# Performance work log

Hardware: AMD Instinct MI355X
Metric: run time of the kernel (lower is better)

The kernel has to match this reference:

```python
import jax, jax.numpy as jnp
import numpy as np

N = 50000   # nodes
E = 800000  # edges
H = 3       # attention heads
IN_F = 128
HID = 128
NUM_CLASSES = 6
GAT_SLOPE = 0.2   # DGL GATConv internal leaky_relu slope
ACT_SLOPE = 0.01  # nn.LeakyReLU default


def setup_inputs() -> dict:
    key = jax.random.key(0)
    ks = jax.random.split(key, 24)
    s = 0.05
    inp = {
        "in_feat": jax.random.normal(ks[0], (N, IN_F), jnp.float32),
        "src": jax.random.randint(ks[1], (E,), 0, N, jnp.int32),
        "dst": jax.random.randint(ks[2], (E,), 0, N, jnp.int32),
        # GATConv 1: W (IN_F, H*HID), attn vectors (H, HID), bias (H*HID)
        "W1": jax.random.normal(ks[3], (IN_F, H * HID), jnp.float32) * s,
        "al1": jax.random.normal(ks[4], (H, HID), jnp.float32) * s,
        "ar1": jax.random.normal(ks[5], (H, HID), jnp.float32) * s,
        "b1": jnp.zeros((H * HID,), jnp.float32),
        # GATConv 2
        "W2": jax.random.normal(ks[6], (HID, H * HID), jnp.float32) * s,
        "al2": jax.random.normal(ks[7], (H, HID), jnp.float32) * s,
        "ar2": jax.random.normal(ks[8], (H, HID), jnp.float32) * s,
        "b2": jnp.zeros((H * HID,), jnp.float32),
    }
    # Dense MLP head lin1..lin4 (HID->HID) and lin5 (HID->NUM_CLASSES)
    for i in range(1, 5):
        inp[f"lw{i}"] = jax.random.normal(ks[8 + 2 * i], (HID, HID), jnp.float32) * s
        inp[f"lb{i}"] = jnp.zeros((HID,), jnp.float32)
    inp["lw5"] = jax.random.normal(ks[20], (HID, NUM_CLASSES), jnp.float32) * s
    inp["lb5"] = jnp.zeros((NUM_CLASSES,), jnp.float32)
    return inp


def gat_conv(x, src, dst, W, al, ar, b):
    # x: (N, F_in) -> out: (N, H, HID)
    h = (x @ W).reshape(N, H, HID)
    el = jnp.einsum('nhf,hf->nh', h, al)  # (N, H)
    er = jnp.einsum('nhf,hf->nh', h, ar)
    e = jax.nn.leaky_relu(el[src] + er[dst], GAT_SLOPE)  # (E, H)
    # edge softmax over incoming edges of each dst node
    m = jax.ops.segment_max(e, dst, num_segments=N)
    m = jnp.where(jnp.isfinite(m), m, 0.0)
    ex = jnp.exp(e - m[dst])
    denom = jax.ops.segment_sum(ex, dst, num_segments=N)
    alpha = ex / (denom[dst] + 1e-9)  # (E, H)
    out = jax.ops.segment_sum(alpha[:, :, None] * h[src], dst, num_segments=N)
    return out + b.reshape(1, H, HID)


def reference(in_feat, src, dst, W1, al1, ar1, b1, W2, al2, ar2, b2,
              lw1, lb1, lw2, lb2, lw3, lb3, lw4, lb4, lw5, lb5):
    act = lambda x: jax.nn.leaky_relu(x, ACT_SLOPE)
    h = act(gat_conv(in_feat, src, dst, W1, al1, ar1, b1)).mean(axis=1)
    h = act(gat_conv(h, src, dst, W2, al2, ar2, b2)).mean(axis=1)
    h = act(h @ lw1 + lb1)
    h = act(h @ lw2 + lb2)
    h = act(h @ lw3 + lb3)
    h = act(h @ lw4 + lb4)
    return h @ lw5 + lb5
```

## Files before the change

kernel.cpp:

```cpp
#include <hip/hip_runtime.h>
#include <hip/hip_bf16.h>


typedef __attribute__((ext_vector_type(8))) short short8;
typedef __attribute__((ext_vector_type(4))) float float4v;

__device__ inline short f2bf(float x) {
    union { float f; unsigned u; } v; v.f = x;
    unsigned r = v.u + 0x7FFFu + ((v.u >> 16) & 1u);
    return (short)(r >> 16);
}
__device__ inline float bf2f(short b) {
    union { float f; unsigned u; } v;
    v.u = ((unsigned)(unsigned short)b) << 16;
    return v.f;
}
__device__ inline float bfhi(unsigned u) {
    union { unsigned u; float f; } v; v.u = u & 0xffff0000u; return v.f;
}
__device__ inline float bflo(unsigned u) {
    union { unsigned u; float f; } v; v.u = u << 16; return v.f;
}
__device__ inline short8 zero8() { short8 z = {0,0,0,0,0,0,0,0}; return z; }

#define BM 128
#define BN 128
#define BK 32
#define LSTR 40
#define MSTR 136
#define MROWS 64

__global__ void prep_kernel(
    const float* __restrict__ in_feat, short* __restrict__ P1h,
    short* __restrict__ P1l, int n4, int cb, int wb,
    const int* __restrict__ dst, int* __restrict__ cnt, int E,
    const float* __restrict__ w1, const float* __restrict__ w2,
    const float* __restrict__ m1, const float* __restrict__ m2,
    const float* __restrict__ m3, const float* __restrict__ m4,
    const float* __restrict__ w5,
    short* __restrict__ w1h, short* __restrict__ w1l,
    short* __restrict__ w2h, short* __restrict__ w2l,
    short* __restrict__ m1h, short* __restrict__ m1l,
    short* __restrict__ m2h, short* __restrict__ m2l,
    short* __restrict__ m3h, short* __restrict__ m3l,
    short* __restrict__ m4h, short* __restrict__ m4l,
    short* __restrict__ w5h, short* __restrict__ w5l)
{
    int blk = blockIdx.x;
    if (blk < cb) {
        int i = blk * 256 + threadIdx.x;
        if (i >= n4) return;
        float4 v = *(const float4*)(in_feat + (size_t)i * 4);
        float xs[4] = {v.x, v.y, v.z, v.w};
        short hs[4], ls[4];
        #pragma unroll
        for (int j = 0; j < 4; ++j) {
            hs[j] = f2bf(xs[j]);
            ls[j] = f2bf(xs[j] - bf2f(hs[j]));
        }
        *(uint2*)(P1h + (size_t)i * 4) = *(uint2*)hs;
        *(uint2*)(P1l + (size_t)i * 4) = *(uint2*)ls;
    } else if (blk < cb + wb) {
        int j = (blk - cb) * 256 + threadIdx.x;
        const float* src; short* th; short* tl; int Nc, base;
        if      (j < 49152)  { src = w1; th = w1h; tl = w1l; Nc = 384; base = 0; }
        else if (j < 98304)  { src = w2; th = w2h; tl = w2l; Nc = 384; base = 49152; }
        else if (j < 114688) { src = m1; th = m1h; tl = m1l; Nc = 128; base = 98304; }
        else if (j < 131072) { src = m2; th = m2h; tl = m2l; Nc = 128; base = 114688; }
        else if (j < 147456) { src = m3; th = m3h; tl = m3l; Nc = 128; base = 131072; }
        else if (j < 163840) { src = m4; th = m4h; tl = m4l; Nc = 128; base = 147456; }
        else if (j < 164608) { src = w5; th = w5h; tl = w5l; Nc = 6;   base = 163840; }
        else return;
        int i = j - base;
        int k = i / Nc, c = i - k * Nc;
        float v = src[i];
        short h = f2bf(v);
        th[(size_t)c * 128 + k] = h;
        tl[(size_t)c * 128 + k] = f2bf(v - bf2f(h));
    } else {
        int e = (blk - cb - wb) * 256 + threadIdx.x;
        if (e < E) atomicAdd(&cnt[dst[e]], 1);
    }
}

__global__ __launch_bounds__(256) void gemm_mfma(
    const short* __restrict__ Ahi, const short* __restrict__ Alo,
    const short* __restrict__ Bth, const short* __restrict__ Btl,
    const float* __restrict__ bias,
    float* __restrict__ Cf, short* __restrict__ Chi, short* __restrict__ Clo,
    float* __restrict__ el, float* __restrict__ er,
    const float* __restrict__ al, const float* __restrict__ ar,
    int M, int Nc, int flags)
{
    __shared__ short Ah[BM * LSTR], Al_[BM * LSTR];
    __shared__ short Bh[BN * LSTR], Bl_[BN * LSTR];

    int tid = threadIdx.x, lane = tid & 63, wave = tid >> 6;
    int l15 = lane & 15, q = lane >> 4;
    int rowBase = blockIdx.y * BM, colBase = blockIdx.x * BN;

    float4v acc[2][8];
    #pragma unroll
    for (int mt = 0; mt < 2; ++mt)
        #pragma unroll
        for (int nt = 0; nt < 8; ++nt)
            acc[mt][nt] = (float4v){0.f, 0.f, 0.f, 0.f};

    for (int k0 = 0; k0 < 128; k0 += BK) {
        #pragma unroll
        for (int s = 0; s < 2; ++s) {
            int c = tid + s * 256;
            int r = c >> 2, kq = (c & 3) * 8;
            int gr = rowBase + r;
            short8 vh = zero8(), vl = zero8();
            if (gr < M) {
                vh = *(const short8*)(Ahi + (size_t)gr * 128 + k0 + kq);
                vl = *(const short8*)(Alo + (size_t)gr * 128 + k0 + kq);
            }
            *(short8*)&Ah[r * LSTR + kq]  = vh;
            *(short8*)&Al_[r * LSTR + kq] = vl;
            int gc = colBase + r;
            short8 wh = zero8(), wl = zero8();
            if (gc < Nc) {
                wh = *(const short8*)(Bth + (size_t)gc * 128 + k0 + kq);
                wl = *(const short8*)(Btl + (size_t)gc * 128 + k0 + kq);
            }
            *(short8*)&Bh[r * LSTR + kq]  = wh;
            *(short8*)&Bl_[r * LSTR + kq] = wl;
        }
        __syncthreads();

        short8 aH[2], aL2[2];
        #pragma unroll
        for (int mt = 0; mt < 2; ++mt) {
            int off = (wave * 32 + mt * 16 + l15) * LSTR + q * 8;
            aH[mt]  = *(short8*)&Ah[off];
            aL2[mt] = *(short8*)&Al_[off];
        }
        #pragma unroll
        for (int nt = 0; nt < 8; ++nt) {
            int off = (nt * 16 + l15) * LSTR + q * 8;
            short8 bH = *(short8*)&Bh[off];
            short8 bL = *(short8*)&Bl_[off];
            #pragma unroll
            for (int mt = 0; mt < 2; ++mt) {
                acc[mt][nt] = __builtin_amdgcn_mfma_f32_16x16x32_bf16(aH[mt], bH, acc[mt][nt], 0, 0, 0);
                acc[mt][nt] = __builtin_amdgcn_mfma_f32_16x16x32_bf16(aH[mt], bL, acc[mt][nt], 0, 0, 0);
                acc[mt][nt] = __builtin_amdgcn_mfma_f32_16x16x32_bf16(aL2[mt], bH, acc[mt][nt], 0, 0, 0);
            }
        }
        __syncthreads();
    }

    if (flags & 4) {
        const float* alh = al + colBase;
        const float* arh = ar + colBase;
        float pel[2][4] = {}, per_[2][4] = {};
        #pragma unroll
        for (int nt = 0; nt < 8; ++nt) {
            float av = alh[nt * 16 + l15];
            float rv = arh[nt * 16 + l15];
            #pragma unroll
            for (int mt = 0; mt < 2; ++mt)
                #pragma unroll
                for (int i = 0; i < 4; ++i) {
                    pel[mt][i]  += acc[mt][nt][i] * av;
                    per_[mt][i] += acc[mt][nt][i] * rv;
                }
        }
        #pragma unroll
        for (int mask = 1; mask < 16; mask <<= 1)
            #pragma unroll
            for (int mt = 0; mt < 2; ++mt)
                #pragma unroll
                for (int i = 0; i < 4; ++i) {
                    pel[mt][i]  += __shfl_xor(pel[mt][i], mask);
                    per_[mt][i] += __shfl_xor(per_[mt][i], mask);
                }
        if (l15 == 0) {
            #pragma unroll
            for (int mt = 0; mt < 2; ++mt)
                #pragma unroll
                for (int i = 0; i < 4; ++i) {
                    int r = rowBase + wave * 32 + mt * 16 + q * 4 + i;
                    if (r < M) {
                        el[r * 3 + blockIdx.x] = pel[mt][i];
                        er[r * 3 + blockIdx.x] = per_[mt][i];
                    }
                }
        }
    }

    #pragma unroll
    for (int mt = 0; mt < 2; ++mt) {
        #pragma unroll
        for (int nt = 0; nt < 8; ++nt) {
            int c = colBase + nt * 16 + l15;
            if (c >= Nc) continue;
            float bv = (flags & 1) ? bias[c] : 0.f;
            #pragma unroll
            for (int i = 0; i < 4; ++i) {
                int r = rowBase + wave * 32 + mt * 16 + q * 4 + i;
                if (r >= M) continue;
                float v = acc[mt][nt][i] + bv;
                if (flags & 2) v = (v < 0.f) ? 0.01f * v : v;
                if (flags & 8)  Cf[(size_t)r * Nc + c] = v;
                if (flags & 16) {
                    size_t idx = (flags & 64)
                        ? ((size_t)r * 128 + (size_t)(c - colBase)) * 3 + blockIdx.x
                        : (size_t)r * Nc + c;
                    short hh = f2bf(v);
                    Chi[idx] = hh;
                    if (flags & 32) Clo[idx] = f2bf(v - bf2f(hh));
                }
            }
        }
    }
}

__global__ __launch_bounds__(256) void mlp_fused(
    const short* __restrict__ Ph, const short* __restrict__ Pl,
    const short* __restrict__ w1h, const short* __restrict__ w1l,
    const short* __restrict__ w2h, const short* __restrict__ w2l,
    const short* __restrict__ w3h, const short* __restrict__ w3l,
    const short* __restrict__ w4h, const short* __restrict__ w4l,
    const short* __restrict__ w5h, const short* __restrict__ w5l,
    const float* __restrict__ b1, const float* __restrict__ b2,
    const float* __restrict__ b3, const float* __restrict__ b4,
    const float* __restrict__ b5,
    float* __restrict__ out, int M)
{
    __shared__ short AH[MROWS * MSTR], AL[MROWS * MSTR];
    __shared__ short WH[128 * LSTR], WL[128 * LSTR];

    int tid = threadIdx.x, lane = tid & 63, wave = tid >> 6;
    int l15 = lane & 15, q = lane >> 4;
    int rowBase = blockIdx.x * MROWS;

    #pragma unroll
    for (int s = 0; s < 4; ++s) {
        int idx = tid + s * 256;
        int r = idx >> 4, kq = (idx & 15) * 8;
        int gr = rowBase + r;
        short8 vh = zero8(), vl = zero8();
        if (gr < M) {
            vh = *(const short8*)(Ph + (size_t)gr * 128 + kq);
            vl = *(const short8*)(Pl + (size_t)gr * 128 + kq);
        }
        *(short8*)&AH[r * MSTR + kq] = vh;
        *(short8*)&AL[r * MSTR + kq] = vl;
    }

    const short* Whs[4] = {w1h, w2h, w3h, w4h};
    const short* Wls[4] = {w1l, w2l, w3l, w4l};
    const float* Bss[4] = {b1, b2, b3, b4};

    #pragma unroll
    for (int L = 0; L < 4; ++L) {
        float4v acc[8];
        #pragma unroll
        for (int nt = 0; nt < 8; ++nt)
            acc[nt] = (float4v){0.f, 0.f, 0.f, 0.f};

        for (int k0 = 0; k0 < 128; k0 += BK) {
            #pragma unroll
            for (int s = 0; s < 4; ++s) {
                int idx = tid + s * 256;
                int plane = idx >> 9, rem = idx & 511;
                int c = rem >> 2, kq = (rem & 3) * 8;
                short8 v = *(const short8*)((plane ? Wls[L] : Whs[L]) +
                                            (size_t)c * 128 + k0 + kq);
                *(short8*)&((plane ? WL : WH)[c * LSTR + kq]) = v;
            }
            __syncthreads();
            int offa = (wave * 16 + l15) * MSTR + k0 + q * 8;
            short8 aH  = *(short8*)&AH[offa];
            short8 aL2 = *(short8*)&AL[offa];
            #pragma unroll
            for (int nt = 0; nt < 8; ++nt) {
                int off = (nt * 16 + l15) * LSTR + q * 8;
                short8 bH = *(short8*)&WH[off];
                short8 bL = *(short8*)&WL[off];
                acc[nt] = __builtin_amdgcn_mfma_f32_16x16x32_bf16(aH, bH, acc[nt], 0, 0, 0);
                acc[nt] = __builtin_amdgcn_mfma_f32_16x16x32_bf16(aH, bL, acc[nt], 0, 0, 0);
                acc[nt] = __builtin_amdgcn_mfma_f32_16x16x32_bf16(aL2, bH, acc[nt], 0, 0, 0);
            }
            __syncthreads();
        }
        #pragma unroll
        for (int nt = 0; nt < 8; ++nt) {
            int c = nt * 16 + l15;
            float bv = Bss[L][c];
            #pragma unroll
            for (int i = 0; i < 4; ++i) {
                int r = wave * 16 + q * 4 + i;
                float v = acc[nt][i] + bv;
                v = (v < 0.f) ? 0.01f * v : v;
                short hh = f2bf(v);
                AH[r * MSTR + c] = hh;
                AL[r * MSTR + c] = f2bf(v - bf2f(hh));
            }
        }
        __syncthreads();
    }

    float4v acc5 = (float4v){0.f, 0.f, 0.f, 0.f};
    for (int k0 = 0; k0 < 128; k0 += BK) {
        if (tid < 128) {
            int plane = tid >> 6, rem = tid & 63;
            int c = rem >> 2, kq = (rem & 3) * 8;
            short8 v = zero8();
            if (c < 6)
                v = *(const short8*)((plane ? w5l : w5h) + (size_t)c * 128 + k0 + kq);
            *(short8*)&((plane ? WL : WH)[c * LSTR + kq]) = v;
        }
        __syncthreads();
        int offa = (wave * 16 + l15) * MSTR + k0 + q * 8;
        short8 aH  = *(short8*)&AH[offa];
        short8 aL2 = *(short8*)&AL[offa];
        int offb = l15 * LSTR + q * 8;
        short8 bH = *(short8*)&WH[offb];
        short8 bL = *(short8*)&WL[offb];
        acc5 = __builtin_amdgcn_mfma_f32_16x16x32_bf16(aH, bH, acc5, 0, 0, 0);
        acc5 = __builtin_amdgcn_mfma_f32_16x16x32_bf16(aH, bL, acc5, 0, 0, 0);
        acc5 = __builtin_amdgcn_mfma_f32_16x16x32_bf16(aL2, bH, acc5, 0, 0, 0);
        __syncthreads();
    }
    if (l15 < 6) {
        float bv = b5[l15];
        #pragma unroll
        for (int i = 0; i < 4; ++i) {
            int r = rowBase + wave * 16 + q * 4 + i;
            if (r < M) out[(size_t)r * 6 + l15] = acc5[i] + bv;
        }
    }
}

__global__ __launch_bounds__(1024) void scan_block(const int* __restrict__ cnt,
                                                   int* __restrict__ off,
                                                   int* __restrict__ bsum, int n)
{
    __shared__ int tmp[1024];
    int tid = threadIdx.x;
    int i = blockIdx.x * 1024 + tid;
    int v = (i < n) ? cnt[i] : 0;
    tmp[tid] = v;
    __syncthreads();
    for (int s = 1; s < 1024; s <<= 1) {
        int t = (tid >= s) ? tmp[tid - s] : 0;
        __syncthreads();
        tmp[tid] += t;
        __syncthreads();
    }
    if (i < n) off[i] = tmp[tid] - v;
    if (tid == 1023) bsum[blockIdx.x] = tmp[1023];
}

__global__ void scan_add2(int* __restrict__ off, const int* __restrict__ bsum,
                          int n, int nb)
{
    __shared__ int pre[64];
    int tid = threadIdx.x;
    if (tid < 64) {
        int v = (tid < nb) ? bsum[tid] : 0;
        #pragma unroll
        for (int s = 1; s < 64; s <<= 1) {
            int t = __shfl_up(v, s);
            if (tid >= s) v += t;
        }
        pre[tid] = v;
    }
    __syncthreads();
    int i = blockIdx.x * blockDim.x + tid;
    if (i < n) {
        int chunk = i >> 10;
        off[i] += chunk ? pre[chunk - 1] : 0;
    }
    if (i == 0) off[n] = pre[nb - 1];
}

__global__ void scatter_kernel(const int* __restrict__ src, const int* __restrict__ dst,
                               const int* __restrict__ off, int* __restrict__ cnt,
                               int* __restrict__ csrc, int E)
{
    int e = blockIdx.x * blockDim.x + threadIdx.x;
    if (e < E) {
        int d = dst[e];
        int p = atomicSub(&cnt[d], 1) - 1;
        csrc[off[d] + p] = src[e];
    }
}

__global__ __launch_bounds__(256) void agg_kernel(
    const short* __restrict__ h, const float* __restrict__ el,
    const float* __restrict__ er, const int* __restrict__ off,
    const int* __restrict__ csrc, const float* __restrict__ bias,
    short* __restrict__ outH, short* __restrict__ outL, int N)
{
    int w = threadIdx.x >> 6;
    int l = threadIdx.x & 63;
    int n = blockIdx.x * 4 + w;
    if (n >= N) return;

    __shared__ int   ssrc[4][64];
    __shared__ float sw3[4][64][3];

    int beg = off[n], end = off[n + 1];
    int deg = end - beg;
    float er0 = er[n * 3 + 0], er1 = er[n * 3 + 1], er2 = er[n * 3 + 2];

    float a00 = 0.f, a01 = 0.f, a02 = 0.f;
    float a10 = 0.f, a11 = 0.f, a12 = 0.f;
    float den0 = 0.f, den1 = 0.f, den2 = 0.f;
    float m0 = -1e30f, m1 = -1e30f, m2 = -1e30f;

    for (int base = 0; base < deg; base += 64) {
        int cnt = min(64, deg - base);
        if (l < cnt) ssrc[w][l] = csrc[beg + base + l];
        float e0 = -1e30f, e1 = -1e30f, e2 = -1e30f;
        if (l < cnt) {
            const float* ep = el + (size_t)ssrc[w][l] * 3;
            float t0 = ep[0] + er0, t1 = ep[1] + er1, t2 = ep[2] + er2;
            e0 = (t0 < 0.f) ? 0.2f * t0 : t0;
            e1 = (t1 < 0.f) ? 0.2f * t1 : t1;
            e2 = (t2 < 0.f) ? 0.2f * t2 : t2;
        }
        float c0 = e0, c1 = e1, c2 = e2;
        #pragma unroll
        for (int msk = 1; msk < 64; msk <<= 1) {
            c0 = fmaxf(c0, __shfl_xor(c0, msk));
            c1 = fmaxf(c1, __shfl_xor(c1, msk));
            c2 = fmaxf(c2, __shfl_xor(c2, msk));
        }
        float n0 = fmaxf(m0, c0), n1 = fmaxf(m1, c1), n2 = fmaxf(m2, c2);
        float s0 = __expf(m0 - n0), s1 = __expf(m1 - n1), s2 = __expf(m2 - n2);
        a00 *= s0; a01 *= s1; a02 *= s2;
        a10 *= s0; a11 *= s1; a12 *= s2;
        den0 *= s0; den1 *= s1; den2 *= s2;
        float w0 = (l < cnt) ? __expf(e0 - n0) : 0.f;
        float w1 = (l < cnt) ? __expf(e1 - n1) : 0.f;
        float w2 = (l < cnt) ? __expf(e2 - n2) : 0.f;
        float ws0 = w0, ws1 = w1, ws2 = w2;
        #pragma unroll
        for (int msk = 1; msk < 64; msk <<= 1) {
            ws0 += __shfl_xor(ws0, msk);
            ws1 += __shfl_xor(ws1, msk);
            ws2 += __shfl_xor(ws2, msk);
        }
        den0 += ws0; den1 += ws1; den2 += ws2;
        sw3[w][l][0] = w0; sw3[w][l][1] = w1; sw3[w][l][2] = w2;
        m0 = n0; m1 = n1; m2 = n2;
        #pragma unroll 4
        for (int qq = 0; qq < cnt; ++qq) {
            int s = ssrc[w][qq];
            float q0 = sw3[w][qq][0], q1 = sw3[w][qq][1], q2 = sw3[w][qq][2];
            uint3 v = *(const uint3*)(h + (size_t)s * 384 + l * 6);
            a00 += q0 * bflo(v.x); a01 += q1 * bfhi(v.x); a02 += q2 * bflo(v.y);
            a10 += q0 * bfhi(v.y); a11 += q1 * bflo(v.z); a12 += q2 * bfhi(v.z);
        }
    }
    float r0 = 1.f / (den0 + 1e-9f), r1 = 1.f / (den1 + 1e-9f), r2 = 1.f / (den2 + 1e-9f);
    if (deg == 0) { r0 = r1 = r2 = 0.f; }
    int f0 = 2 * l, f1 = 2 * l + 1;
    float b00 = bias[f0], b01 = bias[128 + f0], b02 = bias[256 + f0];
    float b10 = bias[f1], b11 = bias[128 + f1], b12 = bias[256 + f1];
    float v00 = a00 * r0 + b00; v00 = (v00 < 0.f) ? 0.01f * v00 : v00;
    float v01 = a01 * r1 + b01; v01 = (v01 < 0.f) ? 0.01f * v01 : v01;
    float v02 = a02 * r2 + b02; v02 = (v02 < 0.f) ? 0.01f * v02 : v02;
    float v10 = a10 * r0 + b10; v10 = (v10 < 0.f) ? 0.01f * v10 : v10;
    float v11 = a11 * r1 + b11; v11 = (v11 < 0.f) ? 0.01f * v11 : v11;
    float v12 = a12 * r2 + b12; v12 = (v12 < 0.f) ? 0.01f * v12 : v12;
    float mx = (v00 + v01 + v02) * (1.0f / 3.0f);
    float my = (v10 + v11 + v12) * (1.0f / 3.0f);
    short hx = f2bf(mx), lx = f2bf(mx - bf2f(hx));
    short hy = f2bf(my), ly = f2bf(my - bf2f(hy));
    unsigned ph = (unsigned)(unsigned short)hx | ((unsigned)(unsigned short)hy << 16);
    unsigned pl = (unsigned)(unsigned short)lx | ((unsigned)(unsigned short)ly << 16);
    *(unsigned*)(outH + (size_t)n * 128 + f0) = ph;
    *(unsigned*)(outL + (size_t)n * 128 + f0) = pl;
}

extern "C" void kernel_launch(void* const* d_in, const int* in_sizes, int n_in,
                              void* d_out, int out_size, void* d_ws, size_t ws_size,
                              hipStream_t stream)
{
    const float* in_feat = (const float*)d_in[0];
    const int*   src     = (const int*)d_in[1];
    const int*   dst     = (const int*)d_in[2];
    const float* W1  = (const float*)d_in[3];
    const float* al1 = (const float*)d_in[4];
    const float* ar1 = (const float*)d_in[5];
    const float* b1  = (const float*)d_in[6];
    const float* W2  = (const float*)d_in[7];
    const float* al2 = (const float*)d_in[8];
    const float* ar2 = (const float*)d_in[9];
    const float* b2  = (const float*)d_in[10];
    const float* lw1 = (const float*)d_in[11];
    const float* lb1 = (const float*)d_in[12];
    const float* lw2 = (const float*)d_in[13];
    const float* lb2 = (const float*)d_in[14];
    const float* lw3 = (const float*)d_in[15];
    const float* lb3 = (const float*)d_in[16];
    const float* lw4 = (const float*)d_in[17];
    const float* lb4 = (const float*)d_in[18];
    const float* lw5 = (const float*)d_in[19];
    const float* lb5 = (const float*)d_in[20];

    const int N = in_sizes[0] / 128;
    const int E = in_sizes[1];

    size_t o = 0;
    auto alloc = [&](size_t bytes) { size_t p = o; o = (o + bytes + 255) & ~(size_t)255; return p; };
    char* ws = (char*)d_ws;
    short* P1h = (short*)(ws + alloc((size_t)N * 128 * 2));
    short* P1l = (short*)(ws + alloc((size_t)N * 128 * 2));
    short* P2h = (short*)(ws + alloc((size_t)N * 128 * 2));
    short* P2l = (short*)(ws + alloc((size_t)N * 128 * 2));
    short* AbH = (short*)(ws + alloc((size_t)N * 384 * 2));
    float* el  = (float*)(ws + alloc((size_t)N * 3 * 4));
    float* er  = (float*)(ws + alloc((size_t)N * 3 * 4));
    int*   cnt  = (int*)(ws + alloc((size_t)N * 4));
    int*   off  = (int*)(ws + alloc((size_t)(N + 1) * 4));
    int*   bsum = (int*)(ws + alloc((size_t)4096));
    int*   csrc = (int*)(ws + alloc((size_t)E * 4));
    short* w1th = (short*)(ws + alloc((size_t)384 * 128 * 2));
    short* w1tl = (short*)(ws + alloc((size_t)384 * 128 * 2));
    short* w2th = (short*)(ws + alloc((size_t)384 * 128 * 2));
    short* w2tl = (short*)(ws + alloc((size_t)384 * 128 * 2));
    short* l1th = (short*)(ws + alloc((size_t)128 * 128 * 2));
    short* l1tl = (short*)(ws + alloc((size_t)128 * 128 * 2));
    short* l2th = (short*)(ws + alloc((size_t)128 * 128 * 2));
    short* l2tl = (short*)(ws + alloc((size_t)128 * 128 * 2));
    short* l3th = (short*)(ws + alloc((size_t)128 * 128 * 2));
    short* l3tl = (short*)(ws + alloc((size_t)128 * 128 * 2));
    short* l4th = (short*)(ws + alloc((size_t)128 * 128 * 2));
    short* l4tl = (short*)(ws + alloc((size_t)128 * 128 * 2));
    short* l5th = (short*)(ws + alloc((size_t)6 * 128 * 2));
    short* l5tl = (short*)(ws + alloc((size_t)6 * 128 * 2));
    (void)ws_size;

    float* out = (float*)d_out;

    hipMemsetAsync(cnt, 0, (size_t)N * 4, stream);
    int n4 = N * 128 / 4;
    int cb = (n4 + 255) / 256;
    int wb = (164608 + 255) / 256;
    int hb = (E + 255) / 256;
    prep_kernel<<<cb + wb + hb, 256, 0, stream>>>(
        in_feat, P1h, P1l, n4, cb, wb, dst, cnt, E,
        W1, W2, lw1, lw2, lw3, lw4, lw5,
        w1th, w1tl, w2th, w2tl, l1th, l1tl, l2th, l2tl,
        l3th, l3tl, l4th, l4tl, l5th, l5tl);

    int nb = (N + 1023) / 1024;
    scan_block<<<nb, 1024, 0, stream>>>(cnt, off, bsum, N);
    scan_add2<<<(N + 255) / 256, 256, 0, stream>>>(off, bsum, N, nb);
    scatter_kernel<<<(E + 255) / 256, 256, 0, stream>>>(src, dst, off, cnt, csrc, E);

    int RB = (N + BM - 1) / BM;
    auto gemm = [&](const short* ah, const short* alo, const short* bth, const short* btl,
                    const float* bias, float* cf, short* chi, short* clo,
                    float* elp, float* erp, const float* alp, const float* arp,
                    int Nc, int flags) {
        dim3 grid((Nc + BN - 1) / BN, RB);
        gemm_mfma<<<grid, 256, 0, stream>>>(ah, alo, bth, btl, bias, cf, chi, clo,
                                            elp, erp, alp, arp, N, Nc, flags);
    };
    int aggGrid = (N + 3) / 4;

    gemm(P1h, P1l, w1th, w1tl, nullptr, nullptr, AbH, nullptr, el, er, al1, ar1, 384, 4 | 16 | 64);
    agg_kernel<<<aggGrid, 256, 0, stream>>>(AbH, el, er, off, csrc, b1, P2h, P2l, N);

    gemm(P2h, P2l, w2th, w2tl, nullptr, nullptr, AbH, nullptr, el, er, al2, ar2, 384, 4 | 16 | 64);
    agg_kernel<<<aggGrid, 256, 0, stream>>>(AbH, el, er, off, csrc, b2, P1h, P1l, N);

    int RBM = (N + MROWS - 1) / MROWS;
    mlp_fused<<<RBM, 256, 0, stream>>>(P1h, P1l,
                                       l1th, l1tl, l2th, l2tl, l3th, l3tl,
                                       l4th, l4tl, l5th, l5tl,
                                       lb1, lb2, lb3, lb4, lb5, out, N);
}
```

Measured before the change: 567.8 us.

## Sort nodes by in-degree so aggregation waves process similar-degree nodes

Builds a degree histogram during the scan pass, prefix-sums it in descending degree order, and writes a permutation of nodes sorted by degree. The aggregation kernel then maps each wave to a node through this permutation, so waves in the same block have similar edge counts and heavy nodes are scheduled first. This targets load imbalance among the four waves of a block. The cost is an extra histogram atomic per node, a small scan kernel, an extra permutation pass, and less locality in output writes, since neighbouring waves now handle non-adjacent node ids.

```diff
diff --git a/kernel.cpp b/kernel.cpp
--- a/kernel.cpp
+++ b/kernel.cpp
@@ -357,6 +357,7 @@
 }
 
 __global__ void scan_add2(int* __restrict__ off, const int* __restrict__ bsum,
+                          const int* __restrict__ cnt, int* __restrict__ dhist,
                           int n, int nb)
 {
     __shared__ int pre[64];
@@ -375,32 +376,63 @@
     if (i < n) {
         int chunk = i >> 10;
         off[i] += chunk ? pre[chunk - 1] : 0;
+        atomicAdd(&dhist[min(cnt[i], 255)], 1);
     }
     if (i == 0) off[n] = pre[nb - 1];
+}
+
+__global__ __launch_bounds__(256) void dscan_kernel(const int* __restrict__ dhist,
+                                                    int* __restrict__ dbase)
+{
+    __shared__ int tmp[256];
+    int tid = threadIdx.x;
+    tmp[tid] = dhist[255 - tid];
+    __syncthreads();
+    for (int s = 1; s < 256; s <<= 1) {
+        int t = (tid >= s) ? tmp[tid - s] : 0;
+        __syncthreads();
+        tmp[tid] += t;
+        __syncthreads();
+    }
+    int bin = 255 - tid;
+    dbase[bin] = tmp[tid] - dhist[bin];
 }
 
 __global__ void scatter_kernel(const int* __restrict__ src, const int* __restrict__ dst,
                                const int* __restrict__ off, int* __restrict__ cnt,
-                               int* __restrict__ csrc, int E)
-{
-    int e = blockIdx.x * blockDim.x + threadIdx.x;
-    if (e < E) {
-        int d = dst[e];
-        int p = atomicSub(&cnt[d], 1) - 1;
-        csrc[off[d] + p] = src[e];
+                               int* __restrict__ csrc, int E, int eb,
+                               int* __restrict__ dbase, int* __restrict__ perm, int N)
+{
+    int blk = blockIdx.x;
+    if (blk < eb) {
+        int e = blk * 256 + threadIdx.x;
+        if (e < E) {
+            int d = dst[e];
+            int p = atomicSub(&cnt[d], 1) - 1;
+            csrc[off[d] + p] = src[e];
+        }
+    } else {
+        int i = (blk - eb) * 256 + threadIdx.x;
+        if (i < N) {
+            int deg = off[i + 1] - off[i];
+            int pos = atomicAdd(&dbase[min(deg, 255)], 1);
+            perm[pos] = i;
+        }
     }
 }
 
 __global__ __launch_bounds__(256) void agg_kernel(
     const short* __restrict__ h, const float* __restrict__ el,
     const float* __restrict__ er, const int* __restrict__ off,
-    const int* __restrict__ csrc, const float* __restrict__ bias,
+    const int* __restrict__ csrc, const int* __restrict__ perm,
+    const float* __restrict__ bias,
     short* __restrict__ outH, short* __restrict__ outL, int N)
 {
     int w = threadIdx.x >> 6;
     int l = threadIdx.x & 63;
-    int n = blockIdx.x * 4 + w;
-    if (n >= N) return;
+    int idx = blockIdx.x * 4 + w;
+    if (idx >= N) return;
+    int n = perm[idx];
 
     __shared__ int   ssrc[4][64];
     __shared__ float sw3[4][64][3];
@@ -519,7 +551,10 @@
     short* AbH = (short*)(ws + alloc((size_t)N * 384 * 2));
     float* el  = (float*)(ws + alloc((size_t)N * 3 * 4));
     float* er  = (float*)(ws + alloc((size_t)N * 3 * 4));
-    int*   cnt  = (int*)(ws + alloc((size_t)N * 4));
+    int*   cnt   = (int*)(ws + alloc((size_t)N * 4));
+    int*   dhist = (int*)(ws + alloc((size_t)256 * 4));
+    int*   dbase = (int*)(ws + alloc((size_t)256 * 4));
+    int*   perm  = (int*)(ws + alloc((size_t)N * 4));
     int*   off  = (int*)(ws + alloc((size_t)(N + 1) * 4));
     int*   bsum = (int*)(ws + alloc((size_t)4096));
     int*   csrc = (int*)(ws + alloc((size_t)E * 4));
@@ -541,7 +576,7 @@
 
     float* out = (float*)d_out;
 
-    hipMemsetAsync(cnt, 0, (size_t)N * 4, stream);
+    hipMemsetAsync(cnt, 0, (size_t)((char*)(dhist + 256) - (char*)cnt), stream);
     int n4 = N * 128 / 4;
     int cb = (n4 + 255) / 256;
     int wb = (164608 + 255) / 256;
@@ -554,8 +589,12 @@
 
     int nb = (N + 1023) / 1024;
     scan_block<<<nb, 1024, 0, stream>>>(cnt, off, bsum, N);
-    scan_add2<<<(N + 255) / 256, 256, 0, stream>>>(off, bsum, N, nb);
-    scatter_kernel<<<(E + 255) / 256, 256, 0, stream>>>(src, dst, off, cnt, csrc, E);
+    scan_add2<<<(N + 255) / 256, 256, 0, stream>>>(off, bsum, cnt, dhist, N, nb);
+    dscan_kernel<<<1, 256, 0, stream>>>(dhist, dbase);
+    int eb = (E + 255) / 256;
+    int pb = (N + 255) / 256;
+    scatter_kernel<<<eb + pb, 256, 0, stream>>>(src, dst, off, cnt, csrc, E, eb,
+                                                dbase, perm, N);
 
     int RB = (N + BM - 1) / BM;
     auto gemm = [&](const short* ah, const short* alo, const short* bth, const short* btl,
@@ -569,10 +608,10 @@
     int aggGrid = (N + 3) / 4;
 
     gemm(P1h, P1l, w1th, w1tl, nullptr, nullptr, AbH, nullptr, el, er, al1, ar1, 384, 4 | 16 | 64);
-    agg_kernel<<<aggGrid, 256, 0, stream>>>(AbH, el, er, off, csrc, b1, P2h, P2l, N);
+    agg_kernel<<<aggGrid, 256, 0, stream>>>(AbH, el, er, off, csrc, perm, b1, P2h, P2l, N);
 
     gemm(P2h, P2l, w2th, w2tl, nullptr, nullptr, AbH, nullptr, el, er, al2, ar2, 384, 4 | 16 | 64);
-    agg_kernel<<<aggGrid, 256, 0, stream>>>(AbH, el, er, off, csrc, b2, P1h, P1l, N);
+    agg_kernel<<<aggGrid, 256, 0, stream>>>(AbH, el, er, off, csrc, perm, b2, P1h, P1l, N);
 
     int RBM = (N + MROWS - 1) / MROWS;
     mlp_fused<<<RBM, 256, 0, stream>>>(P1h, P1l,
```

Result: slower. 831.8 us (+46.5%).
